# Kernel tuning notes

Measured on AMD Instinct MI355X. Metric: run time of the kernel, lower is better.

Reference implementation:

```python
import jax, jax.numpy as jnp
import numpy as np
from jax.scipy.special import logsumexp

EPS_OT = 0.05      # self.eps in AttentionOT
MAX_ITER = 100     # Sinkhorn max_iter (torch early-stops; at convergence results match)


def _l2norm(x):
    # F.normalize(x, dim=-1, p=2) with eps=1e-12
    return x / jnp.maximum(jnp.linalg.norm(x, axis=-1, keepdims=True), 1e-12)


def _sinkhorn(Cmat, mu, nu, eps):
    # Cmat: (BK, M, N), mu: (BK, M), nu: (BK, N)
    log_mu = jnp.log(mu + 1e-8)
    log_nu = jnp.log(nu + 1e-8)

    def kern(u, v):
        # log Boltzmann kernel: (-C + u_i + v_j) / eps, shape (BK, M, N)
        return (-Cmat + u[..., :, None] + v[..., None, :]) / eps

    def step(carry, _):
        u, v = carry
        u = eps * (log_mu - logsumexp(kern(u, v), axis=2)) + u
        v = eps * (log_nu - logsumexp(kern(u, v), axis=1)) + v
        return (u, v), None

    u0 = jnp.zeros_like(mu)
    v0 = jnp.zeros_like(nu)
    (u, v), _ = jax.lax.scan(jax.checkpoint(step), (u0, v0), None, length=MAX_ITER)
    return jnp.exp(kern(u, v))  # transport plan T, (BK, M, N)


def setup_inputs() -> dict:
    key = jax.random.key(0)
    Nq, M, B, K, C = 64, 16, 8, 256, 512
    ks = jax.random.split(key, 8)
    s = 1.0 / np.sqrt(C)  # torch nn.Linear default init bound
    return {
        "xq": jax.random.normal(ks[0], (Nq, M, B, C), jnp.float32),
        "xk": jax.random.normal(ks[1], (B, K, C), jnp.float32),
        "xv": jax.random.normal(ks[2], (B, K, C), jnp.float32),
        "Wq": jax.random.uniform(ks[3], (C, C), jnp.float32, -s, s),
        "Wk": jax.random.uniform(ks[4], (C, C), jnp.float32, -s, s),
        "Wv": jax.random.uniform(ks[5], (C, C), jnp.float32, -s, s),
        "Wp": jax.random.uniform(ks[6], (C, C), jnp.float32, -s, s),
        "bp": jax.random.uniform(ks[7], (C,), jnp.float32, -s, s),
    }


def reference(xq, xk, xv, Wq, Wk, Wv, Wp, bp):
    Nq, M, B, C = xq.shape
    K = xk.shape[1]
    # projections (qkv_bias=False; proj has bias). dropout probs are 0 -> identity.
    q = _l2norm(xq @ Wq.T)          # (Nq, M, B, C)
    kk = _l2norm(xk @ Wk.T)         # (B, K, C)
    v = xv @ Wv.T                   # (B, K, C)
    # torch: einsum('bkc,nmbc->bnkm') then permute(0,2,3,1) -> (B,K,M,Nq)
    sim = jnp.einsum('bkc,nmbc->bkmn', kk, q).reshape(B * K, M, Nq)
    wdist = 1.0 - sim
    mu = jnp.full((B * K, M), 1.0 / M, dtype=sim.dtype)
    nu = jnp.full((B * K, Nq), 1.0 / Nq, dtype=sim.dtype)
    T = _sinkhorn(wdist, mu, nu, EPS_OT)            # (B*K, M, Nq)
    score_map = (M * Nq * sim * T).reshape(B, K, M, Nq)
    attn = T.reshape(B, K, M, Nq).transpose(3, 0, 1, 2)  # (Nq, B, K, M)
    x = jnp.einsum('nbkm,bkc->nmbc', attn, v)            # (Nq, M, B, C)
    x = x @ Wp.T + bp
    return x, score_map
```

## Files before the change

### kernel.cpp

```cpp
#include <hip/hip_runtime.h>


typedef short   short8  __attribute__((ext_vector_type(8)));
typedef float   floatx4 __attribute__((ext_vector_type(4)));
typedef unsigned int uint2e __attribute__((ext_vector_type(2)));

static __device__ __forceinline__ float fastrcp(float x) {
    return __builtin_amdgcn_rcpf(x);
}
static __device__ __forceinline__ unsigned short f2bf(float f) {
    union { float f; unsigned u; } c; c.f = f;
    unsigned r = c.u + 0x7FFF + ((c.u >> 16) & 1);
    return (unsigned short)(r >> 16);
}
static __device__ __forceinline__ float bf2f(unsigned short h) {
    union { unsigned u; float f; } c; c.u = (unsigned)h << 16;
    return c.f;
}

#if __has_builtin(__builtin_amdgcn_permlane16_swap)
static __device__ __forceinline__ float xadd16(float s) {
    uint2e r = __builtin_amdgcn_permlane16_swap(
        __float_as_uint(s), __float_as_uint(s), false, false);
    return __uint_as_float(r.x) + __uint_as_float(r.y);
}
#else
static __device__ __forceinline__ float xadd16(float s) {
    return s + __shfl_xor(s, 16, 64);
}
#endif
#if __has_builtin(__builtin_amdgcn_permlane32_swap)
static __device__ __forceinline__ float xadd32(float s) {
    uint2e r = __builtin_amdgcn_permlane32_swap(
        __float_as_uint(s), __float_as_uint(s), false, false);
    return __uint_as_float(r.x) + __uint_as_float(r.y);
}
#else
static __device__ __forceinline__ float xadd32(float s) {
    return s + __shfl_xor(s, 32, 64);
}
#endif

#define RRI(x, C) __builtin_amdgcn_update_dpp(0, (x), (C), 0xf, 0xf, true)
#define RRF(x, C) __int_as_float(RRI(__float_as_int(x), (C)))
#define GATH16(d, s) do { d[0] = (s);                                        \
    d[1]  = RRF((s), 0x121); d[2]  = RRF((s), 0x122);                        \
    d[3]  = RRF((s), 0x123); d[4]  = RRF((s), 0x124);                        \
    d[5]  = RRF((s), 0x125); d[6]  = RRF((s), 0x126);                        \
    d[7]  = RRF((s), 0x127); d[8]  = RRF((s), 0x128);                        \
    d[9]  = RRF((s), 0x129); d[10] = RRF((s), 0x12a);                        \
    d[11] = RRF((s), 0x12b); d[12] = RRF((s), 0x12c);                        \
    d[13] = RRF((s), 0x12d); d[14] = RRF((s), 0x12e);                        \
    d[15] = RRF((s), 0x12f); } while (0)

__global__ __launch_bounds__(256) void prep(
    const float* __restrict__ xq, const float* __restrict__ xk,
    const float* __restrict__ xv, const float* __restrict__ Wq,
    const float* __restrict__ Wk, const float* __restrict__ Wv,
    const float* __restrict__ Wp,
    unsigned short* __restrict__ xqh, unsigned short* __restrict__ xql,
    unsigned short* __restrict__ xkh, unsigned short* __restrict__ xkl,
    unsigned short* __restrict__ xvb,
    unsigned short* __restrict__ wqh, unsigned short* __restrict__ wql,
    unsigned short* __restrict__ wkh, unsigned short* __restrict__ wkl,
    unsigned short* __restrict__ wvb, unsigned short* __restrict__ wpb)
{
    const int b = blockIdx.x;
    const float* src; unsigned short *dh, *dl; long base;
    if (b < 4096)      { src = xq; dh = xqh; dl = xql;     base = (long)b * 256; }
    else if (b < 5120) { src = xk; dh = xkh; dl = xkl;     base = (long)(b - 4096) * 256; }
    else if (b < 6144) { src = xv; dh = xvb; dl = nullptr; base = (long)(b - 5120) * 256; }
    else if (b < 6400) { src = Wq; dh = wqh; dl = wql;     base = (long)(b - 6144) * 256; }
    else if (b < 6656) { src = Wk; dh = wkh; dl = wkl;     base = (long)(b - 6400) * 256; }
    else if (b < 6912) { src = Wv; dh = wvb; dl = nullptr; base = (long)(b - 6656) * 256; }
    else               { src = Wp; dh = wpb; dl = nullptr; base = (long)(b - 6912) * 256; }
    const long i = base + threadIdx.x;
    float4 v = ((const float4*)src)[i];
    ushort4 h;
    h.x = f2bf(v.x); h.y = f2bf(v.y); h.z = f2bf(v.z); h.w = f2bf(v.w);
    ((ushort4*)dh)[i] = h;
    if (dl) {
        ushort4 l;
        l.x = f2bf(v.x - bf2f(h.x)); l.y = f2bf(v.y - bf2f(h.y));
        l.z = f2bf(v.z - bf2f(h.z)); l.w = f2bf(v.w - bf2f(h.w));
        ((ushort4*)dl)[i] = l;
    }
}

__global__ __launch_bounds__(256) void gemm_qkv2(
    const unsigned short* __restrict__ xqh, const unsigned short* __restrict__ xql,
    const unsigned short* __restrict__ xkh, const unsigned short* __restrict__ xkl,
    const unsigned short* __restrict__ xvb,
    const unsigned short* __restrict__ wqh, const unsigned short* __restrict__ wql,
    const unsigned short* __restrict__ wkh, const unsigned short* __restrict__ wkl,
    const unsigned short* __restrict__ wvb,
    unsigned short* __restrict__ qh, unsigned short* __restrict__ ql,
    unsigned short* __restrict__ kh, unsigned short* __restrict__ kl,
    unsigned short* __restrict__ vt)
{
    __shared__ __align__(16) short LB[20480];
    short (*Ash)[40] = (short(*)[40])(LB);
    short (*Asl)[40] = (short(*)[40])(LB + 5120);
    short (*Bsh)[40] = (short(*)[40])(LB + 10240);
    short (*Bsl)[40] = (short(*)[40])(LB + 15360);

    const int bx = blockIdx.x;
    const unsigned short *Ah, *Al, *Bh, *Bl;
    int seg, arow0;
    if (bx < 64)      { Ah = xqh; Al = xql; Bh = wqh; Bl = wql; arow0 = bx * 128;        seg = 0; }
    else if (bx < 80) { Ah = xkh; Al = xkl; Bh = wkh; Bl = wkl; arow0 = (bx - 64) * 128; seg = 1; }
    else              { Ah = xvb; Al = xvb; Bh = wvb; Bl = wvb; arow0 = (bx - 80) * 128; seg = 2; }
    const bool split = (seg != 2);

    const int tid  = threadIdx.x;
    const int lane = tid & 63, wv = tid >> 6;
    const int wr = (wv >> 1) * 64, wc = (wv & 1) * 64;
    const int j0 = blockIdx.y * 128;

    floatx4 acc[4][4];
#pragma unroll
    for (int i = 0; i < 4; i++)
#pragma unroll
        for (int j = 0; j < 4; j++) acc[i][j] = {0.f, 0.f, 0.f, 0.f};

    const int sr = tid >> 2, sch = (tid & 3) * 8;
    const int fr = lane & 15, fq = (lane >> 4) * 8;

    for (int k0 = 0; k0 < 512; k0 += 32) {
#pragma unroll
        for (int p = 0; p < 2; p++) {
            const int r = sr + p * 64;
            const long ao = (long)(arow0 + r) * 512 + k0 + sch;
            const long bo = (long)(j0 + r) * 512 + k0 + sch;
            *(short8*)&Ash[r][sch] = *(const short8*)(Ah + ao);
            *(short8*)&Bsh[r][sch] = *(const short8*)(Bh + bo);
            if (split) {
                *(short8*)&Asl[r][sch] = *(const short8*)(Al + ao);
                *(short8*)&Bsl[r][sch] = *(const short8*)(Bl + bo);
            }
        }
        __syncthreads();
        short8 ah[4], bh[4];
#pragma unroll
        for (int i = 0; i < 4; i++) ah[i] = *(const short8*)&Ash[wr + i * 16 + fr][fq];
#pragma unroll
        for (int j = 0; j < 4; j++) bh[j] = *(const short8*)&Bsh[wc + j * 16 + fr][fq];
        if (split) {
            short8 al[4], bl[4];
#pragma unroll
            for (int i = 0; i < 4; i++) al[i] = *(const short8*)&Asl[wr + i * 16 + fr][fq];
#pragma unroll
            for (int j = 0; j < 4; j++) bl[j] = *(const short8*)&Bsl[wc + j * 16 + fr][fq];
#pragma unroll
            for (int i = 0; i < 4; i++)
#pragma unroll
                for (int j = 0; j < 4; j++) {
                    acc[i][j] = __builtin_amdgcn_mfma_f32_16x16x32_bf16(ah[i], bh[j], acc[i][j], 0, 0, 0);
                    acc[i][j] = __builtin_amdgcn_mfma_f32_16x16x32_bf16(ah[i], bl[j], acc[i][j], 0, 0, 0);
                    acc[i][j] = __builtin_amdgcn_mfma_f32_16x16x32_bf16(al[i], bh[j], acc[i][j], 0, 0, 0);
                }
        } else {
#pragma unroll
            for (int i = 0; i < 4; i++)
#pragma unroll
                for (int j = 0; j < 4; j++)
                    acc[i][j] = __builtin_amdgcn_mfma_f32_16x16x32_bf16(ah[i], bh[j], acc[i][j], 0, 0, 0);
        }
        __syncthreads();
    }

    const int cr = (lane >> 4) * 4, cc = lane & 15;
    if (seg == 2) {
        short (*S2)[136] = (short(*)[136])LB;
#pragma unroll
        for (int i = 0; i < 4; i++)
#pragma unroll
            for (int j = 0; j < 4; j++)
#pragma unroll
                for (int r = 0; r < 4; r++)
                    S2[wc + j * 16 + cc][wr + i * 16 + cr + r] =
                        (short)f2bf(acc[i][j][r]);
        __syncthreads();
        const int orow = tid >> 1;
        const int os   = (tid & 1) * 64;
        unsigned short* dst = vt + (long)(arow0 >> 8) * 131072
                            + (long)(j0 + orow) * 256 + (arow0 & 255) + os;
#pragma unroll
        for (int c8 = 0; c8 < 8; c8++)
            *(short8*)(dst + c8 * 8) = *(const short8*)&S2[orow][os + c8 * 8];
    } else {
#pragma unroll
        for (int i = 0; i < 4; i++)
#pragma unroll
            for (int j = 0; j < 4; j++) {
                const int gj = j0 + wc + j * 16 + cc;
#pragma unroll
                for (int r = 0; r < 4; r++) {
                    const int gi = arow0 + wr + i * 16 + cr + r;
                    const float v = acc[i][j][r];
                    const unsigned short h = f2bf(v);
                    const unsigned short lo = f2bf(v - bf2f(h));
                    if (seg == 0) {
                        const long orow = (long)((gi & 7) * 1024 + ((gi >> 3) & 15) * 64 + (gi >> 7));
                        qh[orow * 512 + gj] = h;
                        ql[orow * 512 + gj] = lo;
                    } else {
                        kh[(long)gi * 512 + gj] = h;
                        kl[(long)gi * 512 + gj] = lo;
                    }
                }
            }
    }
}

__global__ __launch_bounds__(256) void gemm_sim64(
    const short* __restrict__ Ah, const short* __restrict__ Al,
    const short* __restrict__ Bh, const short* __restrict__ Bl,
    float* __restrict__ Out, const float* __restrict__ rs)
{
    const int z = blockIdx.z;
    Ah += (long)z * 131072;  Al += (long)z * 131072;
    Bh += (long)z * 524288;  Bl += (long)z * 524288;
    Out += (long)z * 262144;
    const float* rsq = rs + (long)z * 1024;
    const float* rsk = rs + 8192 + (long)z * 256;

    __shared__ __align__(16) short Ash[64][40];
    __shared__ __align__(16) short Asl[64][40];
    __shared__ __align__(16) short Bsh[64][40];
    __shared__ __align__(16) short Bsl[64][40];

    const int tid  = threadIdx.x;
    const int lane = tid & 63, wv = tid >> 6;
    const int wr = (wv >> 1) * 32, wc = (wv & 1) * 32;
    const int i0 = blockIdx.x * 64, j0 = blockIdx.y * 64;

    floatx4 acc[2][2];
#pragma unroll
    for (int i = 0; i < 2; i++)
#pragma unroll
        for (int j = 0; j < 2; j++) acc[i][j] = {0.f, 0.f, 0.f, 0.f};

    const int sr = tid >> 2, sch = (tid & 3) * 8;
    const int fr = lane & 15, fq = (lane >> 4) * 8;

    for (int k0 = 0; k0 < 512; k0 += 32) {
        const long ao = (long)(i0 + sr) * 512 + k0 + sch;
        const long bo = (long)(j0 + sr) * 512 + k0 + sch;
        *(short8*)&Ash[sr][sch] = *(const short8*)(Ah + ao);
        *(short8*)&Asl[sr][sch] = *(const short8*)(Al + ao);
        *(short8*)&Bsh[sr][sch] = *(const short8*)(Bh + bo);
        *(short8*)&Bsl[sr][sch] = *(const short8*)(Bl + bo);
        __syncthreads();
        short8 ah[2], al[2], bh[2], bl[2];
#pragma unroll
        for (int i = 0; i < 2; i++) {
            ah[i] = *(const short8*)&Ash[wr + i * 16 + fr][fq];
            al[i] = *(const short8*)&Asl[wr + i * 16 + fr][fq];
        }
#pragma unroll
        for (int j = 0; j < 2; j++) {
            bh[j] = *(const short8*)&Bsh[wc + j * 16 + fr][fq];
            bl[j] = *(const short8*)&Bsl[wc + j * 16 + fr][fq];
        }
#pragma unroll
        for (int i = 0; i < 2; i++)
#pragma unroll
            for (int j = 0; j < 2; j++) {
                acc[i][j] = __builtin_amdgcn_mfma_f32_16x16x32_bf16(ah[i], bh[j], acc[i][j], 0, 0, 0);
                acc[i][j] = __builtin_amdgcn_mfma_f32_16x16x32_bf16(ah[i], bl[j], acc[i][j], 0, 0, 0);
                acc[i][j] = __builtin_amdgcn_mfma_f32_16x16x32_bf16(al[i], bh[j], acc[i][j], 0, 0, 0);
            }
        __syncthreads();
    }

    const int cr = (lane >> 4) * 4, cc = lane & 15;
#pragma unroll
    for (int i = 0; i < 2; i++)
#pragma unroll
        for (int j = 0; j < 2; j++) {
            const int gj = j0 + wc + j * 16 + cc;
            const float sq = rsq[gj];
#pragma unroll
            for (int r = 0; r < 4; r++) {
                const int gi = i0 + wr + i * 16 + cr + r;
                Out[(long)gi * 1024 + gj] = acc[i][j][r] * rsk[gi] * sq;
            }
        }
}

template <bool BIAS, bool OPERM, bool OUT_BF16>
__global__ __launch_bounds__(256) void gemm_bf16(
    const short* __restrict__ A, const short* __restrict__ B,
    const float* __restrict__ bias, void* __restrict__ OutV,
    int Kdim, int lda, int ldb, int ldo, long sA, long sB, long sO)
{
    __shared__ __align__(16) short As[128][40];
    __shared__ __align__(16) short Bs[128][40];

    const int tid  = threadIdx.x;
    const int lane = tid & 63, wv = tid >> 6;
    const int wr = (wv >> 1) * 64, wc = (wv & 1) * 64;
    const int i0 = blockIdx.x * 128, j0 = blockIdx.y * 128;

    floatx4 acc[4][4];
#pragma unroll
    for (int i = 0; i < 4; i++)
#pragma unroll
        for (int j = 0; j < 4; j++) acc[i][j] = {0.f, 0.f, 0.f, 0.f};

    const int sr = tid >> 2, sk = (tid & 3) * 8;
    const int fr = lane & 15, fq = (lane >> 4) * 8;
    const short* pa = A + (long)blockIdx.z * sA;
    const short* pb = B + (long)blockIdx.z * sB;

    for (int k0 = 0; k0 < Kdim; k0 += 32) {
#pragma unroll
        for (int p = 0; p < 2; p++) {
            *(short8*)&As[sr + p * 64][sk] =
                *(const short8*)(pa + (long)(i0 + sr + p * 64) * lda + k0 + sk);
            *(short8*)&Bs[sr + p * 64][sk] =
                *(const short8*)(pb + (long)(j0 + sr + p * 64) * ldb + k0 + sk);
        }
        __syncthreads();
        short8 af[4], bf[4];
#pragma unroll
        for (int i = 0; i < 4; i++) af[i] = *(const short8*)&As[wr + i * 16 + fr][fq];
#pragma unroll
        for (int j = 0; j < 4; j++) bf[j] = *(const short8*)&Bs[wc + j * 16 + fr][fq];
#pragma unroll
        for (int i = 0; i < 4; i++)
#pragma unroll
            for (int j = 0; j < 4; j++)
                acc[i][j] = __builtin_amdgcn_mfma_f32_16x16x32_bf16(af[i], bf[j], acc[i][j], 0, 0, 0);
        __syncthreads();
    }

    float* Of = nullptr; unsigned short* Ob = nullptr;
    if constexpr (OUT_BF16) Ob = (unsigned short*)OutV + (long)blockIdx.z * sO;
    else                    Of = (float*)OutV + (long)blockIdx.z * sO;
    const int cr = (lane >> 4) * 4, cc = lane & 15;
#pragma unroll
    for (int i = 0; i < 4; i++) {
#pragma unroll
        for (int j = 0; j < 4; j++) {
            const int gj = j0 + wc + j * 16 + cc;
            float bb = 0.0f;
            if constexpr (BIAS) bb = bias[gj];
#pragma unroll
            for (int r = 0; r < 4; r++) {
                const int gi = i0 + wr + i * 16 + cr + r;
                float v = acc[i][j][r] + bb;
                long idx;
                if constexpr (OPERM)
                    idx = (long)((gi & 63) * 128 + ((gi >> 6) & 15) * 8 + (gi >> 10)) * ldo + gj;
                else
                    idx = (long)gi * ldo + gj;
                if constexpr (OUT_BF16) Ob[idx] = f2bf(v);
                else                    Of[idx] = v;
            }
        }
    }
}

__global__ __launch_bounds__(256) void rownorm(
    const unsigned short* __restrict__ qh, const unsigned short* __restrict__ ql,
    const unsigned short* __restrict__ kh, const unsigned short* __restrict__ kl,
    float* __restrict__ rs)
{
    const int row  = blockIdx.x * 4 + (threadIdx.x >> 6);
    const int lane = threadIdx.x & 63;
    const unsigned short *ph, *pl;
    long r;
    if (row < 8192) { ph = qh; pl = ql; r = row; }
    else            { ph = kh; pl = kl; r = row - 8192; }
    const long o = r * 512 + lane * 8;
    ushort4 h0 = *(const ushort4*)(ph + o), h1 = *(const ushort4*)(ph + o + 4);
    ushort4 l0 = *(const ushort4*)(pl + o), l1 = *(const ushort4*)(pl + o + 4);
    float ss = 0.0f;
    const unsigned short hv[8] = {h0.x, h0.y, h0.z, h0.w, h1.x, h1.y, h1.z, h1.w};
    const unsigned short lv[8] = {l0.x, l0.y, l0.z, l0.w, l1.x, l1.y, l1.z, l1.w};
#pragma unroll
    for (int i = 0; i < 8; i++) {
        const float v = bf2f(hv[i]) + bf2f(lv[i]);
        ss = fmaf(v, v, ss);
    }
#pragma unroll
    for (int off = 32; off; off >>= 1) ss += __shfl_xor(ss, off, 64);
    if (lane == 0) rs[row] = 1.0f / fmaxf(sqrtf(ss), 1e-12f);
}

__global__ __launch_bounds__(256, 2) void sinkhorn5(
    const float* __restrict__ sim, float* __restrict__ score,
    unsigned short* __restrict__ Tt)
{
    const int lane = threadIdx.x & 63;
    const int bk   = blockIdx.x * 4 + (threadIdx.x >> 6);
    const float* S = sim + (long)bk * 1024;
    const int m = lane & 15, g = lane >> 4;

    int idx[16];
    idx[0] = m;
    idx[1]  = RRI(m, 0x121); idx[2]  = RRI(m, 0x122); idx[3]  = RRI(m, 0x123);
    idx[4]  = RRI(m, 0x124); idx[5]  = RRI(m, 0x125); idx[6]  = RRI(m, 0x126);
    idx[7]  = RRI(m, 0x127); idx[8]  = RRI(m, 0x128); idx[9]  = RRI(m, 0x129);
    idx[10] = RRI(m, 0x12a); idx[11] = RRI(m, 0x12b); idx[12] = RRI(m, 0x12c);
    idx[13] = RRI(m, 0x12d); idx[14] = RRI(m, 0x12e); idx[15] = RRI(m, 0x12f);

    float K1[16], K2R[16], sv[16];
#pragma unroll
    for (int j = 0; j < 16; j++) {
        K1[j] = __expf((S[m * 64 + g * 16 + idx[j]] - 1.0f) * 20.0f);
        const float s_ = S[idx[j] * 64 + lane];
        sv[j]  = s_;
        K2R[j] = __expf((s_ - 1.0f) * 20.0f);
    }

    const float muP = 0.0625f + 1e-8f;
    const float nuP = 0.015625f + 1e-8f;
    float b = 1.0f;
    float aB[16], bB[16];
#pragma unroll
    for (int j = 0; j < 16; j++) bB[j] = 1.0f;

#pragma unroll 1
    for (int it = 0; it < 100; it++) {
        float s0 = 0, s1 = 0, s2 = 0, s3 = 0;
#pragma unroll
        for (int j = 0; j < 4; j++) {
            s0 = fmaf(K1[j],      bB[j],      s0);
            s1 = fmaf(K1[4 + j],  bB[4 + j],  s1);
            s2 = fmaf(K1[8 + j],  bB[8 + j],  s2);
            s3 = fmaf(K1[12 + j], bB[12 + j], s3);
        }
        float s = (s0 + s1) + (s2 + s3);
        s = xadd16(s);
        s = xadd32(s);
        const float a = muP * fastrcp(s);
        GATH16(aB, a);
        float t0 = 0, t1 = 0, t2 = 0, t3 = 0;
#pragma unroll
        for (int j = 0; j < 4; j++) {
            t0 = fmaf(K2R[j],      aB[j],      t0);
            t1 = fmaf(K2R[4 + j],  aB[4 + j],  t1);
            t2 = fmaf(K2R[8 + j],  aB[8 + j],  t2);
            t3 = fmaf(K2R[12 + j], aB[12 + j], t3);
        }
        const float bp_ = b;
        b = nuP * fastrcp((t0 + t1) + (t2 + t3));
        GATH16(bB, b);
        const int conv = __builtin_fabsf(b - bp_) <= 1e-5f * __builtin_fabsf(b);
        if (__all(conv)) break;
    }

    float* Sc = score + (long)bk * 1024;
    unsigned short* Tp = Tt + (long)(bk >> 8) * 262144 + (bk & 255);
#pragma unroll
    for (int j = 0; j < 16; j++) {
        const int row = idx[j];
        const float Tv = aB[j] * K2R[j] * b;
        Sc[row * 64 + lane] = 1024.0f * sv[j] * Tv;
        Tp[(long)(row * 64 + lane) * 256] = f2bf(Tv);
    }
}

extern "C" void kernel_launch(void* const* d_in, const int* in_sizes, int n_in,
                              void* d_out, int out_size, void* d_ws, size_t ws_size,
                              hipStream_t stream)
{
    (void)in_sizes; (void)n_in; (void)out_size; (void)ws_size;
    const float* xq = (const float*)d_in[0];
    const float* xk = (const float*)d_in[1];
    const float* xv = (const float*)d_in[2];
    const float* Wq = (const float*)d_in[3];
    const float* Wk = (const float*)d_in[4];
    const float* Wv = (const float*)d_in[5];
    const float* Wp = (const float*)d_in[6];
    const float* bp = (const float*)d_in[7];

    float* out_x     = (float*)d_out;
    float* out_score = out_x + 8192L * 512;

    char* W = (char*)d_ws;
    const long MB = 1 << 20;
    unsigned short* qh   = (unsigned short*)(W + 0);
    unsigned short* ql   = (unsigned short*)(W + 8 * MB);
    unsigned short* xq_h = (unsigned short*)(W + 16 * MB);
    float*          simb = (float*)(W + 16 * MB);
    unsigned short* xq_l = (unsigned short*)(W + 24 * MB);
    unsigned short* xpre = (unsigned short*)(W + 24 * MB);
    unsigned short* xk_h = (unsigned short*)(W + 32 * MB);
    unsigned short* xk_l = (unsigned short*)(W + 34 * MB);
    unsigned short* Tt   = (unsigned short*)(W + 32 * MB);
    unsigned short* xv_b = (unsigned short*)(W + 36 * MB);
    unsigned short* kh   = (unsigned short*)(W + 38 * MB);
    unsigned short* kl   = (unsigned short*)(W + 40 * MB);
    unsigned short* vt   = (unsigned short*)(W + 42 * MB);
    unsigned short* wqh  = (unsigned short*)(W + 44 * MB);
    unsigned short* wql  = (unsigned short*)(W + 44 * MB + 1 * 524288);
    unsigned short* wkh  = (unsigned short*)(W + 44 * MB + 2 * 524288);
    unsigned short* wkl  = (unsigned short*)(W + 44 * MB + 3 * 524288);
    unsigned short* wvb  = (unsigned short*)(W + 44 * MB + 4 * 524288);
    unsigned short* wpb  = (unsigned short*)(W + 44 * MB + 5 * 524288);
    float*          rs   = (float*)(W + 47 * MB);

    const dim3 blk(256);

    prep<<<7168, blk, 0, stream>>>(xq, xk, xv, Wq, Wk, Wv, Wp,
                                   xq_h, xq_l, xk_h, xk_l, xv_b,
                                   wqh, wql, wkh, wkl, wvb, wpb);

    gemm_qkv2<<<dim3(96, 4), blk, 0, stream>>>(
        xq_h, xq_l, xk_h, xk_l, xv_b, wqh, wql, wkh, wkl, wvb,
        qh, ql, kh, kl, vt);

    rownorm<<<2560, blk, 0, stream>>>(qh, ql, kh, kl, rs);

    gemm_sim64<<<dim3(4, 16, 8), blk, 0, stream>>>(
        (const short*)kh, (const short*)kl, (const short*)qh, (const short*)ql,
        simb, rs);

    sinkhorn5<<<512, blk, 0, stream>>>(simb, out_score, Tt);

    gemm_bf16<false, false, true><<<dim3(8, 4, 8), blk, 0, stream>>>(
        (const short*)Tt, (const short*)vt, nullptr, xpre,
        256, 256, 256, 512, 262144, 131072, 524288);

    gemm_bf16<true, true, false><<<dim3(64, 4), blk, 0, stream>>>(
        (const short*)xpre, (const short*)wpb, bp, out_x,
        512, 512, 512, 512, 0, 0, 0);
}
```

Baseline: 197.0 us.

## Double-buffer LDS tiles with register prefetch in QKV projection GEMM

The QKV projection GEMM now prefetches the next K-slice from global memory into registers while MFMAs run on the current LDS buffer, then writes it into an alternate LDS buffer. This removes one barrier per iteration and hides global load latency behind compute. In exchange it doubles LDS use to 80KB and adds register pressure. It also sets launch_bounds min-blocks to 2, which may cap registers.

```diff
diff --git a/kernel.cpp b/kernel.cpp
--- a/kernel.cpp
+++ b/kernel.cpp
@@ -87,7 +87,7 @@
     }
 }
 
-__global__ __launch_bounds__(256) void gemm_qkv2(
+__global__ __launch_bounds__(256, 2) void gemm_qkv2(
     const unsigned short* __restrict__ xqh, const unsigned short* __restrict__ xql,
     const unsigned short* __restrict__ xkh, const unsigned short* __restrict__ xkl,
     const unsigned short* __restrict__ xvb,
@@ -98,11 +98,7 @@
     unsigned short* __restrict__ kh, unsigned short* __restrict__ kl,
     unsigned short* __restrict__ vt)
 {
-    __shared__ __align__(16) short LB[20480];
-    short (*Ash)[40] = (short(*)[40])(LB);
-    short (*Asl)[40] = (short(*)[40])(LB + 5120);
-    short (*Bsh)[40] = (short(*)[40])(LB + 10240);
-    short (*Bsl)[40] = (short(*)[40])(LB + 15360);
+    __shared__ __align__(16) short LB[40960];
 
     const int bx = blockIdx.x;
     const unsigned short *Ah, *Al, *Bh, *Bl;
@@ -126,31 +122,60 @@
     const int sr = tid >> 2, sch = (tid & 3) * 8;
     const int fr = lane & 15, fq = (lane >> 4) * 8;
 
-    for (int k0 = 0; k0 < 512; k0 += 32) {
-#pragma unroll
-        for (int p = 0; p < 2; p++) {
-            const int r = sr + p * 64;
-            const long ao = (long)(arow0 + r) * 512 + k0 + sch;
-            const long bo = (long)(j0 + r) * 512 + k0 + sch;
-            *(short8*)&Ash[r][sch] = *(const short8*)(Ah + ao);
-            *(short8*)&Bsh[r][sch] = *(const short8*)(Bh + bo);
-            if (split) {
-                *(short8*)&Asl[r][sch] = *(const short8*)(Al + ao);
-                *(short8*)&Bsl[r][sch] = *(const short8*)(Bl + bo);
-            }
-        }
-        __syncthreads();
+    short8 ra0, ra1, rb0, rb1, rla0, rla1, rlb0, rlb1;
+
+#define QKV_LOADT(k0) do {                                                   \
+        const long ao0 = (long)(arow0 + sr) * 512 + (k0) + sch;              \
+        const long bo0 = (long)(j0 + sr) * 512 + (k0) + sch;                 \
+        ra0 = *(const short8*)(Ah + ao0);                                    \
+        ra1 = *(const short8*)(Ah + ao0 + 64 * 512);                         \
+        rb0 = *(const short8*)(Bh + bo0);                                    \
+        rb1 = *(const short8*)(Bh + bo0 + 64 * 512);                         \
+        if (split) {                                                         \
+            rla0 = *(const short8*)(Al + ao0);                               \
+            rla1 = *(const short8*)(Al + ao0 + 64 * 512);                    \
+            rlb0 = *(const short8*)(Bl + bo0);                               \
+            rlb1 = *(const short8*)(Bl + bo0 + 64 * 512);                    \
+        }                                                                    \
+    } while (0)
+
+#define QKV_WRITET(d) do {                                                   \
+        short* base_ = LB + (d) * 20480;                                     \
+        *(short8*)&base_[sr * 40 + sch]                 = ra0;               \
+        *(short8*)&base_[(sr + 64) * 40 + sch]          = ra1;               \
+        *(short8*)&base_[10240 + sr * 40 + sch]         = rb0;               \
+        *(short8*)&base_[10240 + (sr + 64) * 40 + sch]  = rb1;               \
+        if (split) {                                                         \
+            *(short8*)&base_[5120 + sr * 40 + sch]                = rla0;    \
+            *(short8*)&base_[5120 + (sr + 64) * 40 + sch]         = rla1;    \
+            *(short8*)&base_[15360 + sr * 40 + sch]               = rlb0;    \
+            *(short8*)&base_[15360 + (sr + 64) * 40 + sch]        = rlb1;    \
+        }                                                                    \
+    } while (0)
+
+    QKV_LOADT(0);
+    QKV_WRITET(0);
+    __syncthreads();
+
+#pragma unroll 2
+    for (int t = 0; t < 16; t++) {
+        if (t < 15) QKV_LOADT((t + 1) * 32);
+        const short* base = LB + (t & 1) * 20480;
         short8 ah[4], bh[4];
 #pragma unroll
-        for (int i = 0; i < 4; i++) ah[i] = *(const short8*)&Ash[wr + i * 16 + fr][fq];
-#pragma unroll
-        for (int j = 0; j < 4; j++) bh[j] = *(const short8*)&Bsh[wc + j * 16 + fr][fq];
+        for (int i = 0; i < 4; i++)
+            ah[i] = *(const short8*)&base[(wr + i * 16 + fr) * 40 + fq];
+#pragma unroll
+        for (int j = 0; j < 4; j++)
+            bh[j] = *(const short8*)&base[10240 + (wc + j * 16 + fr) * 40 + fq];
         if (split) {
             short8 al[4], bl[4];
 #pragma unroll
-            for (int i = 0; i < 4; i++) al[i] = *(const short8*)&Asl[wr + i * 16 + fr][fq];
-#pragma unroll
-            for (int j = 0; j < 4; j++) bl[j] = *(const short8*)&Bsl[wc + j * 16 + fr][fq];
+            for (int i = 0; i < 4; i++)
+                al[i] = *(const short8*)&base[5120 + (wr + i * 16 + fr) * 40 + fq];
+#pragma unroll
+            for (int j = 0; j < 4; j++)
+                bl[j] = *(const short8*)&base[15360 + (wc + j * 16 + fr) * 40 + fq];
 #pragma unroll
             for (int i = 0; i < 4; i++)
 #pragma unroll
@@ -166,6 +191,7 @@
                 for (int j = 0; j < 4; j++)
                     acc[i][j] = __builtin_amdgcn_mfma_f32_16x16x32_bf16(ah[i], bh[j], acc[i][j], 0, 0, 0);
         }
+        if (t < 15) QKV_WRITET((t + 1) & 1);
         __syncthreads();
     }
 
@@ -211,6 +237,8 @@
                 }
             }
     }
+#undef QKV_LOADT
+#undef QKV_WRITET
 }
 
 __global__ __launch_bounds__(256) void gemm_sim64(
```

Result: no change. 196.3 us (-0.4%).
